# Kernel optimization log

Measured on AMD Instinct MI355X. Metric: run time of the kernel, lower is better.

## Reference

```python
import jax, jax.numpy as jnp
import numpy as np


def setup_inputs() -> dict:
    key = jax.random.key(0)
    ks = jax.random.split(key, 5)
    B, H, W, C = 64, 14, 14, 2048
    x = jax.random.normal(ks[0], (B, H, W, C), dtype=jnp.float32)
    # Glorot-ish scaled 1x1 conv weights (stored as [Cin, Cout])
    W1 = jax.random.normal(ks[1], (C, 64), dtype=jnp.float32) * (1.0 / np.sqrt(C))
    W2 = jax.random.normal(ks[2], (64, 16), dtype=jnp.float32) * (1.0 / np.sqrt(64))
    W3 = jax.random.normal(ks[3], (16, 8), dtype=jnp.float32) * (1.0 / np.sqrt(16))
    W4 = jax.random.normal(ks[4], (8, 1), dtype=jnp.float32) * (1.0 / np.sqrt(8))
    return {
        "x": x,
        "W1": W1, "b1": jnp.zeros((64,), jnp.float32),
        "W2": W2, "b2": jnp.zeros((16,), jnp.float32),
        "W3": W3, "b3": jnp.zeros((8,), jnp.float32),
        "W4": W4, "b4": jnp.zeros((1,), jnp.float32),
    }


def reference(x, W1, b1, W2, b2, W3, b3, W4, b4):
    # Dropout is identity at inference time.
    # 1x1 convs == per-pixel matmuls over channel dim.
    h = jax.nn.relu(jnp.einsum('bhwc,cd->bhwd', x, W1) + b1)   # [B,H,W,64]
    h = jax.nn.relu(jnp.einsum('bhwc,cd->bhwd', h, W2) + b2)   # [B,H,W,16]
    h = jax.nn.relu(jnp.einsum('bhwc,cd->bhwd', h, W3) + b3)   # [B,H,W,8]
    a = jax.nn.sigmoid(jnp.einsum('bhwc,cd->bhwd', h, W4) + b4)  # [B,H,W,1]
    # 'upsample' frozen ones-conv == broadcast of a over 2048 channels.
    gap_features = jnp.mean(a * x, axis=(1, 2))  # [B, 2048]
    gap_mask = jnp.mean(a, axis=(1, 2))          # [B, 1] (same value for all 2048 chans)
    return gap_features / gap_mask               # [B, 2048]
```

## Files before the change

kernel.cpp:

```cpp
#include <hip/hip_runtime.h>
#include <math.h>

#define NPIX 12544
#define CIN  2048
#define NB   64
#define PPIX 196
#define PSPLIT 14
#define PCHUNK 14

typedef short  bf16x8 __attribute__((ext_vector_type(8)));
typedef float  f32x4  __attribute__((ext_vector_type(4)));

__device__ inline unsigned short f2bf(float f) {
    unsigned int u = __float_as_uint(f);
    u = (u + 0x7fffu + ((u >> 16) & 1u)) >> 16;
    return (unsigned short)u;
}

__global__ __launch_bounds__(256) void conv_w1(
    const float* __restrict__ W1, unsigned short* __restrict__ W1t)
{
    const int id = blockIdx.x * 256 + threadIdx.x;
    const int n = id >> 11;
    const int k = id & 2047;
    W1t[id] = f2bf(W1[k * 64 + n]);
}

__global__ __launch_bounds__(512, 2) void attn_scores_mfma(
    const float* __restrict__ x, const unsigned short* __restrict__ W1t,
    const float* __restrict__ b1,
    const float* __restrict__ W2, const float* __restrict__ b2,
    const float* __restrict__ W3, const float* __restrict__ b3,
    const float* __restrict__ W4, const float* __restrict__ b4,
    float* __restrict__ a_out)
{
    __shared__ float part[8][16][68];
    __shared__ float h1s[16][68];
    __shared__ float h2s[16][16];
    __shared__ float h3s[16][8];

    const int t    = threadIdx.x;
    const int wv   = t >> 6;
    const int lane = t & 63;
    const int l15  = lane & 15;
    const int q    = lane >> 4;
    const size_t pix0 = (size_t)blockIdx.x * 16;

    const float* xr = x + (pix0 + l15) * (size_t)CIN + wv * 256 + q * 8;
    const unsigned short* wr = W1t + (size_t)l15 * CIN + wv * 256 + q * 8;

    f32x4 acc[4] = {{0,0,0,0},{0,0,0,0},{0,0,0,0},{0,0,0,0}};

    float4 xv[16];
#pragma unroll
    for (int i = 0; i < 4; ++i) {
        xv[2*i]   = *(const float4*)(xr + 32*i);
        xv[2*i+1] = *(const float4*)(xr + 32*i + 4);
    }
    bf16x8 wA[4], wB[4];
#pragma unroll
    for (int ct = 0; ct < 4; ++ct)
        wA[ct] = *(const bf16x8*)(wr + (size_t)ct * 16 * CIN);

#pragma unroll
    for (int i = 0; i < 8; ++i) {
        if (i < 4) {
            xv[8+2*i] = *(const float4*)(xr + 32*(i+4));
            xv[9+2*i] = *(const float4*)(xr + 32*(i+4) + 4);
        }
        if (i < 7) {
            if ((i & 1) == 0) {
#pragma unroll
                for (int ct = 0; ct < 4; ++ct)
                    wB[ct] = *(const bf16x8*)(wr + (size_t)ct * 16 * CIN + 32*(i+1));
            } else {
#pragma unroll
                for (int ct = 0; ct < 4; ++ct)
                    wA[ct] = *(const bf16x8*)(wr + (size_t)ct * 16 * CIN + 32*(i+1));
            }
        }
        const float4 xa = xv[(2*i) & 15];
        const float4 xb = xv[(2*i+1) & 15];
        bf16x8 af;
        af[0] = (short)f2bf(xa.x); af[1] = (short)f2bf(xa.y);
        af[2] = (short)f2bf(xa.z); af[3] = (short)f2bf(xa.w);
        af[4] = (short)f2bf(xb.x); af[5] = (short)f2bf(xb.y);
        af[6] = (short)f2bf(xb.z); af[7] = (short)f2bf(xb.w);
        if ((i & 1) == 0) {
#pragma unroll
            for (int ct = 0; ct < 4; ++ct)
                acc[ct] = __builtin_amdgcn_mfma_f32_16x16x32_bf16(af, wA[ct], acc[ct], 0, 0, 0);
        } else {
#pragma unroll
            for (int ct = 0; ct < 4; ++ct)
                acc[ct] = __builtin_amdgcn_mfma_f32_16x16x32_bf16(af, wB[ct], acc[ct], 0, 0, 0);
        }
    }

#pragma unroll
    for (int ct = 0; ct < 4; ++ct)
#pragma unroll
        for (int r = 0; r < 4; ++r)
            part[wv][q * 4 + r][ct * 16 + l15] = acc[ct][r];
    __syncthreads();

    const int p = t >> 4;
    const int j = t & 15;

    if (t < 256) {
        const int c0 = j * 4;
        f32x4 s = {0, 0, 0, 0};
#pragma unroll
        for (int w = 0; w < 8; ++w) s += *(const f32x4*)&part[w][p][c0];
        const f32x4 bb = *(const f32x4*)(b1 + c0);
        f32x4 hv;
#pragma unroll
        for (int i = 0; i < 4; ++i) hv[i] = fmaxf(s[i] + bb[i], 0.f);
        *(f32x4*)&h1s[p][c0] = hv;
    }
    __syncthreads();

    if (t < 256) {
        float s = b2[j];
#pragma unroll
        for (int k = 0; k < 64; ++k) s = fmaf(h1s[p][k], W2[k * 16 + j], s);
        h2s[p][j] = fmaxf(s, 0.f);
    }
    __syncthreads();

    if (t < 256 && j < 8) {
        float s = b3[j];
#pragma unroll
        for (int k = 0; k < 16; ++k) s = fmaf(h2s[p][k], W3[k * 8 + j], s);
        h3s[p][j] = fmaxf(s, 0.f);
    }
    __syncthreads();

    if (t < 256 && j == 0) {
        float z = b4[0];
#pragma unroll
        for (int k = 0; k < 8; ++k) z = fmaf(h3s[p][k], W4[k], z);
        a_out[pix0 + p] = 1.f / (1.f + expf(-z));
    }
}

__global__ __launch_bounds__(256) void gap_partial(
    const float* __restrict__ x, const float* __restrict__ a,
    float* __restrict__ part)
{
    const int b  = blockIdx.y;
    const int pz = blockIdx.z;
    const int c0 = (blockIdx.x * 256 + threadIdx.x) * 4;
    const float* xb = x + ((size_t)b * PPIX + pz * PCHUNK) * CIN + c0;
    const float* ab = a + b * PPIX + pz * PCHUNK;

    float av[PCHUNK];
#pragma unroll
    for (int p = 0; p < PCHUNK; ++p) av[p] = ab[p];

    float4 xv[PCHUNK];
#pragma unroll
    for (int p = 0; p < PCHUNK; ++p)
        xv[p] = *(const float4*)(xb + (size_t)p * CIN);

    float4 s0 = {0,0,0,0}, s1 = {0,0,0,0};
#pragma unroll
    for (int p = 0; p < PCHUNK; p += 2) {
        s0.x = fmaf(av[p], xv[p].x, s0.x);   s0.y = fmaf(av[p], xv[p].y, s0.y);
        s0.z = fmaf(av[p], xv[p].z, s0.z);   s0.w = fmaf(av[p], xv[p].w, s0.w);
        s1.x = fmaf(av[p+1], xv[p+1].x, s1.x); s1.y = fmaf(av[p+1], xv[p+1].y, s1.y);
        s1.z = fmaf(av[p+1], xv[p+1].z, s1.z); s1.w = fmaf(av[p+1], xv[p+1].w, s1.w);
    }
    float4 r;
    r.x = s0.x + s1.x; r.y = s0.y + s1.y; r.z = s0.z + s1.z; r.w = s0.w + s1.w;
    *(float4*)(part + ((size_t)pz * NB + b) * CIN + c0) = r;
}

__global__ __launch_bounds__(512) void gap_final(
    const float* __restrict__ a, const float* __restrict__ part,
    float* __restrict__ out)
{
    __shared__ float red[512];
    const int b = blockIdx.x, t = threadIdx.x;
    red[t] = (t < PPIX) ? a[b * PPIX + t] : 0.f;
    __syncthreads();
#pragma unroll
    for (int s = 256; s > 0; s >>= 1) {
        if (t < s) red[t] += red[t + s];
        __syncthreads();
    }
    const float inv = 1.f / red[0];
    const int c0 = t * 4;
    float4 acc = {0, 0, 0, 0};
#pragma unroll
    for (int z = 0; z < PSPLIT; ++z) {
        const float4 pv = *(const float4*)(part + ((size_t)z * NB + b) * CIN + c0);
        acc.x += pv.x; acc.y += pv.y; acc.z += pv.z; acc.w += pv.w;
    }
    float4 r;
    r.x = acc.x * inv; r.y = acc.y * inv; r.z = acc.z * inv; r.w = acc.w * inv;
    *(float4*)(out + (size_t)b * CIN + c0) = r;
}

extern "C" void kernel_launch(void* const* d_in, const int* in_sizes, int n_in,
                              void* d_out, int out_size, void* d_ws, size_t ws_size,
                              hipStream_t stream)
{
    const float* x  = (const float*)d_in[0];
    const float* W1 = (const float*)d_in[1];
    const float* b1 = (const float*)d_in[2];
    const float* W2 = (const float*)d_in[3];
    const float* b2 = (const float*)d_in[4];
    const float* W3 = (const float*)d_in[5];
    const float* b3 = (const float*)d_in[6];
    const float* W4 = (const float*)d_in[7];
    const float* b4 = (const float*)d_in[8];
    float* out = (float*)d_out;

    unsigned short* W1t = (unsigned short*)d_ws;
    float* a    = (float*)((char*)d_ws + (256 << 10));
    float* part = (float*)((char*)d_ws + (512 << 10));

    conv_w1<<<512, 256, 0, stream>>>(W1, W1t);
    attn_scores_mfma<<<NPIX / 16, 512, 0, stream>>>(x, W1t, b1, W2, b2, W3, b3, W4, b4, a);
    gap_partial<<<dim3(2, NB, PSPLIT), 256, 0, stream>>>(x, a, part);
    gap_final<<<NB, 512, 0, stream>>>(a, part, out);
}
```

Before: 209.4 us.

## Fuse attention scoring and weighted GAP into one kernel via LDS-staged bf16 x

Merges the attention-score MFMA kernel with the weighted pooling kernel: each block stages 14 pixels of x as bf16 in shared memory, computes the MLP attention, then reduces a*x per block directly from shared memory. This avoids reading x from global memory a second time and writing/reading the attention map. The h1 reduction across waves now uses LDS atomics, and per-block partial sums feed a final kernel. It trades precision (pooling uses bf16-rounded x), shuffle-heavy reductions and high LDS usage for less HBM traffic.

```diff
diff --git a/kernel.cpp b/kernel.cpp
--- a/kernel.cpp
+++ b/kernel.cpp
@@ -5,10 +5,12 @@
 #define CIN  2048
 #define NB   64
 #define PPIX 196
-#define PSPLIT 14
-#define PCHUNK 14
+#define BPIMG 14
+#define PXB  14
+#define NBLK (NB * BPIMG)
 
 typedef short  bf16x8 __attribute__((ext_vector_type(8)));
+typedef short  bf16x4 __attribute__((ext_vector_type(4)));
 typedef float  f32x4  __attribute__((ext_vector_type(4)));
 
 __device__ inline unsigned short f2bf(float f) {
@@ -16,6 +18,9 @@
     u = (u + 0x7fffu + ((u >> 16) & 1u)) >> 16;
     return (unsigned short)u;
 }
+__device__ inline float bf2f(unsigned short u) {
+    return __uint_as_float((unsigned int)u << 16);
+}
 
 __global__ __launch_bounds__(256) void conv_w1(
     const float* __restrict__ W1, unsigned short* __restrict__ W1t)
@@ -26,108 +31,104 @@
     W1t[id] = f2bf(W1[k * 64 + n]);
 }
 
-__global__ __launch_bounds__(512, 2) void attn_scores_mfma(
+__global__ __launch_bounds__(512, 4) void fused_attn_gap(
     const float* __restrict__ x, const unsigned short* __restrict__ W1t,
     const float* __restrict__ b1,
     const float* __restrict__ W2, const float* __restrict__ b2,
     const float* __restrict__ W3, const float* __restrict__ b3,
     const float* __restrict__ W4, const float* __restrict__ b4,
-    float* __restrict__ a_out)
-{
-    __shared__ float part[8][16][68];
+    float* __restrict__ part2, float* __restrict__ asum_part)
+{
+    __shared__ short xs[256 * 16 * 8];
     __shared__ float h1s[16][68];
     __shared__ float h2s[16][16];
     __shared__ float h3s[16][8];
+    __shared__ float a_s[16];
 
     const int t    = threadIdx.x;
     const int wv   = t >> 6;
     const int lane = t & 63;
     const int l15  = lane & 15;
     const int q    = lane >> 4;
-    const size_t pix0 = (size_t)blockIdx.x * 16;
-
-    const float* xr = x + (pix0 + l15) * (size_t)CIN + wv * 256 + q * 8;
+    const int blk  = blockIdx.x;
+    const size_t pix0 = (size_t)blk * PXB;
+
+    const int tp = t >> 5;
+    const int tc = t & 31;
+    float4 xv[16];
+    if (tp < PXB) {
+        const float* xp = x + (pix0 + tp) * (size_t)CIN + tc * 4;
+#pragma unroll
+        for (int i = 0; i < 16; ++i)
+            xv[i] = *(const float4*)(xp + i * 128);
+    } else {
+#pragma unroll
+        for (int i = 0; i < 16; ++i) xv[i] = make_float4(0.f, 0.f, 0.f, 0.f);
+    }
+    if (t < 256)
+        *(f32x4*)&h1s[t >> 4][(t & 15) * 4] = *(const f32x4*)(b1 + (t & 15) * 4);
+#pragma unroll
+    for (int i = 0; i < 16; ++i) {
+        const int k = tc * 4 + i * 128;
+        const int g = k >> 3;
+        const int e = k & 7;
+        bf16x4 w;
+        w[0] = (short)f2bf(xv[i].x); w[1] = (short)f2bf(xv[i].y);
+        w[2] = (short)f2bf(xv[i].z); w[3] = (short)f2bf(xv[i].w);
+        *(bf16x4*)&xs[(g * 16 + tp) * 8 + e] = w;
+    }
+    __syncthreads();
+
     const unsigned short* wr = W1t + (size_t)l15 * CIN + wv * 256 + q * 8;
+    const bf16x8* xsv = (const bf16x8*)xs;
+    const int gq = wv * 32 + q;
 
     f32x4 acc[4] = {{0,0,0,0},{0,0,0,0},{0,0,0,0},{0,0,0,0}};
-
-    float4 xv[16];
-#pragma unroll
-    for (int i = 0; i < 4; ++i) {
-        xv[2*i]   = *(const float4*)(xr + 32*i);
-        xv[2*i+1] = *(const float4*)(xr + 32*i + 4);
-    }
     bf16x8 wA[4], wB[4];
 #pragma unroll
     for (int ct = 0; ct < 4; ++ct)
         wA[ct] = *(const bf16x8*)(wr + (size_t)ct * 16 * CIN);
-
 #pragma unroll
     for (int i = 0; i < 8; ++i) {
-        if (i < 4) {
-            xv[8+2*i] = *(const float4*)(xr + 32*(i+4));
-            xv[9+2*i] = *(const float4*)(xr + 32*(i+4) + 4);
-        }
         if (i < 7) {
             if ((i & 1) == 0) {
 #pragma unroll
                 for (int ct = 0; ct < 4; ++ct)
-                    wB[ct] = *(const bf16x8*)(wr + (size_t)ct * 16 * CIN + 32*(i+1));
+                    wB[ct] = *(const bf16x8*)(wr + (size_t)ct * 16 * CIN + 32 * (i + 1));
             } else {
 #pragma unroll
                 for (int ct = 0; ct < 4; ++ct)
-                    wA[ct] = *(const bf16x8*)(wr + (size_t)ct * 16 * CIN + 32*(i+1));
+                    wA[ct] = *(const bf16x8*)(wr + (size_t)ct * 16 * CIN + 32 * (i + 1));
             }
         }
-        const float4 xa = xv[(2*i) & 15];
-        const float4 xb = xv[(2*i+1) & 15];
-        bf16x8 af;
-        af[0] = (short)f2bf(xa.x); af[1] = (short)f2bf(xa.y);
-        af[2] = (short)f2bf(xa.z); af[3] = (short)f2bf(xa.w);
-        af[4] = (short)f2bf(xb.x); af[5] = (short)f2bf(xb.y);
-        af[6] = (short)f2bf(xb.z); af[7] = (short)f2bf(xb.w);
+        const bf16x8 av = xsv[(gq + i * 4) * 16 + l15];
         if ((i & 1) == 0) {
 #pragma unroll
             for (int ct = 0; ct < 4; ++ct)
-                acc[ct] = __builtin_amdgcn_mfma_f32_16x16x32_bf16(af, wA[ct], acc[ct], 0, 0, 0);
+                acc[ct] = __builtin_amdgcn_mfma_f32_16x16x32_bf16(av, wA[ct], acc[ct], 0, 0, 0);
         } else {
 #pragma unroll
             for (int ct = 0; ct < 4; ++ct)
-                acc[ct] = __builtin_amdgcn_mfma_f32_16x16x32_bf16(af, wB[ct], acc[ct], 0, 0, 0);
+                acc[ct] = __builtin_amdgcn_mfma_f32_16x16x32_bf16(av, wB[ct], acc[ct], 0, 0, 0);
         }
     }
-
 #pragma unroll
     for (int ct = 0; ct < 4; ++ct)
 #pragma unroll
         for (int r = 0; r < 4; ++r)
-            part[wv][q * 4 + r][ct * 16 + l15] = acc[ct][r];
+            atomicAdd(&h1s[q * 4 + r][ct * 16 + l15], acc[ct][r]);
     __syncthreads();
 
     const int p = t >> 4;
     const int j = t & 15;
-
-    if (t < 256) {
-        const int c0 = j * 4;
-        f32x4 s = {0, 0, 0, 0};
-#pragma unroll
-        for (int w = 0; w < 8; ++w) s += *(const f32x4*)&part[w][p][c0];
-        const f32x4 bb = *(const f32x4*)(b1 + c0);
-        f32x4 hv;
-#pragma unroll
-        for (int i = 0; i < 4; ++i) hv[i] = fmaxf(s[i] + bb[i], 0.f);
-        *(f32x4*)&h1s[p][c0] = hv;
-    }
-    __syncthreads();
-
     if (t < 256) {
         float s = b2[j];
 #pragma unroll
-        for (int k = 0; k < 64; ++k) s = fmaf(h1s[p][k], W2[k * 16 + j], s);
+        for (int k = 0; k < 64; ++k)
+            s = fmaf(fmaxf(h1s[p][k], 0.f), W2[k * 16 + j], s);
         h2s[p][j] = fmaxf(s, 0.f);
     }
     __syncthreads();
-
     if (t < 256 && j < 8) {
         float s = b3[j];
 #pragma unroll
@@ -135,66 +136,61 @@
         h3s[p][j] = fmaxf(s, 0.f);
     }
     __syncthreads();
-
     if (t < 256 && j == 0) {
         float z = b4[0];
 #pragma unroll
         for (int k = 0; k < 8; ++k) z = fmaf(h3s[p][k], W4[k], z);
-        a_out[pix0 + p] = 1.f / (1.f + expf(-z));
-    }
-}
-
-__global__ __launch_bounds__(256) void gap_partial(
-    const float* __restrict__ x, const float* __restrict__ a,
-    float* __restrict__ part)
-{
-    const int b  = blockIdx.y;
-    const int pz = blockIdx.z;
-    const int c0 = (blockIdx.x * 256 + threadIdx.x) * 4;
-    const float* xb = x + ((size_t)b * PPIX + pz * PCHUNK) * CIN + c0;
-    const float* ab = a + b * PPIX + pz * PCHUNK;
-
-    float av[PCHUNK];
-#pragma unroll
-    for (int p = 0; p < PCHUNK; ++p) av[p] = ab[p];
-
-    float4 xv[PCHUNK];
-#pragma unroll
-    for (int p = 0; p < PCHUNK; ++p)
-        xv[p] = *(const float4*)(xb + (size_t)p * CIN);
-
-    float4 s0 = {0,0,0,0}, s1 = {0,0,0,0};
-#pragma unroll
-    for (int p = 0; p < PCHUNK; p += 2) {
-        s0.x = fmaf(av[p], xv[p].x, s0.x);   s0.y = fmaf(av[p], xv[p].y, s0.y);
-        s0.z = fmaf(av[p], xv[p].z, s0.z);   s0.w = fmaf(av[p], xv[p].w, s0.w);
-        s1.x = fmaf(av[p+1], xv[p+1].x, s1.x); s1.y = fmaf(av[p+1], xv[p+1].y, s1.y);
-        s1.z = fmaf(av[p+1], xv[p+1].z, s1.z); s1.w = fmaf(av[p+1], xv[p+1].w, s1.w);
-    }
-    float4 r;
-    r.x = s0.x + s1.x; r.y = s0.y + s1.y; r.z = s0.z + s1.z; r.w = s0.w + s1.w;
-    *(float4*)(part + ((size_t)pz * NB + b) * CIN + c0) = r;
+        a_s[p] = (p < PXB) ? (1.f / (1.f + expf(-z))) : 0.f;
+    }
+    __syncthreads();
+
+    if (t == 0) {
+        float s = 0.f;
+#pragma unroll
+        for (int pp = 0; pp < PXB; ++pp) s += a_s[pp];
+        asum_part[blk] = s;
+    }
+
+    const float ap = a_s[l15];
+#pragma unroll
+    for (int gi = 0; gi < 8; ++gi) {
+        const int g = wv * 32 + q * 8 + gi;
+        const bf16x8 v = xsv[g * 16 + l15];
+        float sarr[8];
+#pragma unroll
+        for (int e = 0; e < 8; ++e)
+            sarr[e] = ap * bf2f((unsigned short)v[e]);
+#pragma unroll
+        for (int m = 1; m < 16; m <<= 1)
+#pragma unroll
+            for (int e = 0; e < 8; ++e)
+                sarr[e] += __shfl_xor(sarr[e], m, 16);
+        if (l15 == 0) {
+            float* dst = part2 + (size_t)blk * CIN + g * 8;
+            *(float4*)dst       = make_float4(sarr[0], sarr[1], sarr[2], sarr[3]);
+            *(float4*)(dst + 4) = make_float4(sarr[4], sarr[5], sarr[6], sarr[7]);
+        }
+    }
 }
 
 __global__ __launch_bounds__(512) void gap_final(
-    const float* __restrict__ a, const float* __restrict__ part,
+    const float* __restrict__ asum_part, const float* __restrict__ part2,
     float* __restrict__ out)
 {
-    __shared__ float red[512];
+    __shared__ float red[16];
     const int b = blockIdx.x, t = threadIdx.x;
-    red[t] = (t < PPIX) ? a[b * PPIX + t] : 0.f;
-    __syncthreads();
-#pragma unroll
-    for (int s = 256; s > 0; s >>= 1) {
-        if (t < s) red[t] += red[t + s];
-        __syncthreads();
-    }
-    const float inv = 1.f / red[0];
+    if (t < 16) red[t] = (t < BPIMG) ? asum_part[b * BPIMG + t] : 0.f;
+    __syncthreads();
+    float s = 0.f;
+#pragma unroll
+    for (int z = 0; z < BPIMG; ++z) s += red[z];
+    const float inv = 1.f / s;
+
     const int c0 = t * 4;
-    float4 acc = {0, 0, 0, 0};
-#pragma unroll
-    for (int z = 0; z < PSPLIT; ++z) {
-        const float4 pv = *(const float4*)(part + ((size_t)z * NB + b) * CIN + c0);
+    float4 acc = {0.f, 0.f, 0.f, 0.f};
+#pragma unroll
+    for (int z = 0; z < BPIMG; ++z) {
+        const float4 pv = *(const float4*)(part2 + (size_t)(b * BPIMG + z) * CIN + c0);
         acc.x += pv.x; acc.y += pv.y; acc.z += pv.z; acc.w += pv.w;
     }
     float4 r;
@@ -218,11 +214,11 @@
     float* out = (float*)d_out;
 
     unsigned short* W1t = (unsigned short*)d_ws;
-    float* a    = (float*)((char*)d_ws + (256 << 10));
-    float* part = (float*)((char*)d_ws + (512 << 10));
+    float* asum_part = (float*)((char*)d_ws + (512 << 10));
+    float* part2     = (float*)((char*)d_ws + (1 << 20));
 
     conv_w1<<<512, 256, 0, stream>>>(W1, W1t);
-    attn_scores_mfma<<<NPIX / 16, 512, 0, stream>>>(x, W1t, b1, W2, b2, W3, b3, W4, b4, a);
-    gap_partial<<<dim3(2, NB, PSPLIT), 256, 0, stream>>>(x, a, part);
-    gap_final<<<NB, 512, 0, stream>>>(a, part, out);
-}
+    fused_attn_gap<<<NBLK, 512, 0, stream>>>(x, W1t, b1, W2, b2, W3, b3, W4, b4,
+                                             part2, asum_part);
+    gap_final<<<NB, 512, 0, stream>>>(asum_part, part2, out);
+}
```

Result: slower. 235.2 us (+12.3%).
